# Kernel tuning notes

Hardware: AMD Instinct MI355X
Metric: run time of the kernel (lower is better)

## Reference

```python
import jax, jax.numpy as jnp
import numpy as np
from jax import lax


def setup_inputs() -> dict:
    key = jax.random.key(0)
    ks = jax.random.split(key, 6)
    B, T, F, C = 32, 256, 64, 16
    CO, P, S, K = 16, 64, 32, 4
    x = jax.random.normal(ks[0], (B, T, F, C), dtype=jnp.float32)
    static = jax.random.normal(ks[1], (B, S), dtype=jnp.float32)
    conv_w = jax.random.normal(ks[2], (F, CO, C, K), dtype=jnp.float32) * (1.0 / np.sqrt(C * K))
    conv_b = jax.random.normal(ks[3], (F, CO), dtype=jnp.float32) * 0.01
    W_p = jax.random.normal(ks[4], (F * C + S, P), dtype=jnp.float32) * (1.0 / np.sqrt(F * C + S))
    b_p = jax.random.normal(ks[5], (P,), dtype=jnp.float32) * 0.01
    return {"x": x, "static": static, "conv_w": conv_w, "conv_b": conv_b,
            "W_p": W_p, "b_p": b_p, "dilation": 2}


def _tpc_forward(x, static, conv_w, conv_b, W_p, b_p, dilation):
    B, T, F, C = x.shape
    _, CO, _, K = conv_w.shape
    left_pad = dilation * (K - 1)
    # --- feature-wise causal temporal conv as one grouped dilated conv ---
    # [B, T, F, C] -> [B, F*C, T]  (NCH layout)
    xr = x.transpose(0, 2, 3, 1).reshape(B, F * C, T)
    kr = conv_w.reshape(F * CO, C, K)  # groups = F
    y = lax.conv_general_dilated(
        xr, kr,
        window_strides=(1,),
        padding=[(left_pad, 0)],  # causal left padding
        rhs_dilation=(dilation,),
        dimension_numbers=("NCH", "OIH", "NCH"),
        feature_group_count=F,
    )  # [B, F*CO, T]
    temp_out = y.reshape(B, F, CO, T).transpose(0, 3, 1, 2) + conv_b[None, None, :, :]
    # --- pointwise branch on flattened features + static ---
    flat_x = x.reshape(B, T, F * C)
    static_rep = jnp.broadcast_to(static[:, None, :], (B, T, static.shape[-1]))
    point_in = jnp.concatenate([flat_x, static_rep], axis=-1)  # [B, T, F*C+S]
    point_out = point_in @ W_p + b_p  # [B, T, P]
    point_bcast = jnp.broadcast_to(point_out[:, :, None, :], (B, T, F, point_out.shape[-1]))
    # --- concat fusion + ReLU ---
    fused = jnp.concatenate([x, temp_out, point_bcast], axis=-1)
    return jax.nn.relu(fused)


def reference(x, static, conv_w, conv_b, W_p, b_p, dilation):
    return _tpc_forward(x, static, conv_w, conv_b, W_p, b_p, dilation)
```

## Files before the change

### kernel.cpp

```cpp
#include <hip/hip_runtime.h>

#define B_  32
#define T_  256
#define F_  64
#define C_  16
#define CO_ 16
#define P_  64
#define S_  32
#define K_  4
#define FC_ 1024
#define OUTC 96
#define TT  8
#define NS  14

typedef float floatx4 __attribute__((ext_vector_type(4)));

#define BARRIER_LGKM() asm volatile("s_waitcnt lgkmcnt(0)\n\ts_barrier" ::: "memory")

__global__ __launch_bounds__(512, 4) void tpc_fused(
    const float* __restrict__ x, const float* __restrict__ stat,
    const float* __restrict__ cw, const float* __restrict__ cb,
    const float* __restrict__ Wp, const float* __restrict__ bp,
    float* __restrict__ out)
{
    __shared__ __align__(16) float xs[NS * FC_];
    __shared__ __align__(16) float u[4096];

    int tid = threadIdx.x;
    int blk = blockIdx.x;
    int b  = blk >> 5;
    int t0 = (blk & 31) * TT;

    #pragma unroll
    for (int it = 0; it < 7; ++it) {
        int v = it * 512 + tid;
        int slice = v >> 8;
        int pos   = v & 255;
        int tg = t0 - 6 + slice;
        float4 val = make_float4(0.f, 0.f, 0.f, 0.f);
        if (tg >= 0)
            val = *(const float4*)(x + ((size_t)(b * T_ + tg)) * FC_ + pos * 4);
        *(float4*)(xs + slice * FC_ + pos * 4) = val;
    }
    __syncthreads();

    {
        int p  = tid & 63;
        int ks = tid >> 6;
        float acc[TT];
        #pragma unroll
        for (int r = 0; r < TT; ++r) acc[r] = 0.f;
        int k0base = ks * 128;
        for (int kk = 0; kk < 128; kk += 4) {
            int k0 = k0base + kk;
            float w0 = Wp[(size_t)(k0 + 0) * P_ + p];
            float w1 = Wp[(size_t)(k0 + 1) * P_ + p];
            float w2 = Wp[(size_t)(k0 + 2) * P_ + p];
            float w3 = Wp[(size_t)(k0 + 3) * P_ + p];
            #pragma unroll
            for (int r = 0; r < TT; ++r) {
                float4 xv = *(const float4*)(xs + (6 + r) * FC_ + k0);
                acc[r] += xv.x * w0 + xv.y * w1 + xv.z * w2 + xv.w * w3;
            }
        }
        #pragma unroll
        for (int r = 0; r < TT; ++r)
            u[(ks * TT + r) * P_ + p] = acc[r];
    }
    __syncthreads();

    {
        int p = tid & 63;
        int r = tid >> 6;
        float s = bp[p];
        const float* wst = Wp + (size_t)FC_ * P_;
        #pragma unroll 8
        for (int si = 0; si < S_; ++si)
            s += stat[b * S_ + si] * wst[si * P_ + p];
        #pragma unroll
        for (int ks = 0; ks < 8; ++ks)
            s += u[(ks * TT + r) * P_ + p];
        __syncthreads();
        u[3072 + r * P_ + p] = fmaxf(s, 0.f);
    }
    __syncthreads();

    int co = tid & 15;
    int fh = tid >> 4;
    int p  = tid & 63;
    int fg = tid >> 6;

    #pragma unroll
    for (int half = 0; half < 2; ++half) {
        int f = half * 32 + fh;
        float w[64];
        const float4* wg = (const float4*)(cw + ((size_t)(f * CO_ + co)) * (C_ * K_));
        #pragma unroll
        for (int j = 0; j < 16; ++j) {
            float4 t4 = wg[j];
            w[4 * j + 0] = t4.x; w[4 * j + 1] = t4.y;
            w[4 * j + 2] = t4.z; w[4 * j + 3] = t4.w;
        }
        float bias = cb[f * CO_ + co];

        for (int tl = 0; tl < TT; ++tl) {
            float temp = bias;
            #pragma unroll
            for (int k = 0; k < K_; ++k) {
                const float* sp = xs + (tl + 2 * k) * FC_ + f * C_;
                #pragma unroll
                for (int c4 = 0; c4 < 4; ++c4) {
                    float4 xv = *(const float4*)(sp + c4 * 4);
                    temp += xv.x * w[(c4 * 4 + 0) * 4 + k];
                    temp += xv.y * w[(c4 * 4 + 1) * 4 + k];
                    temp += xv.z * w[(c4 * 4 + 2) * 4 + k];
                    temp += xv.w * w[(c4 * 4 + 3) * 4 + k];
                }
            }
            u[fh * OUTC + 16 + co] = fmaxf(temp, 0.f);
            u[fh * OUTC + co] = fmaxf(xs[(tl + 6) * FC_ + f * C_ + co], 0.f);
            float pvv = u[3072 + tl * P_ + p];
            #pragma unroll
            for (int fo = 0; fo < 4; ++fo)
                u[(fo * 8 + fg) * OUTC + 32 + p] = pvv;
            BARRIER_LGKM();
            {
                const floatx4* src = (const floatx4*)u;
                floatx4* dst = (floatx4*)(out + ((size_t)(b * T_ + t0 + tl)) * F_ * OUTC
                                          + half * 3072);
                __builtin_nontemporal_store(src[tid], &dst[tid]);
                if (tid < 256)
                    __builtin_nontemporal_store(src[512 + tid], &dst[512 + tid]);
            }
            BARRIER_LGKM();
        }
    }
}

extern "C" void kernel_launch(void* const* d_in, const int* in_sizes, int n_in,
                              void* d_out, int out_size, void* d_ws, size_t ws_size,
                              hipStream_t stream) {
    const float* x    = (const float*)d_in[0];
    const float* stat = (const float*)d_in[1];
    const float* cw   = (const float*)d_in[2];
    const float* cb   = (const float*)d_in[3];
    const float* Wp   = (const float*)d_in[4];
    const float* bp   = (const float*)d_in[5];
    float* out = (float*)d_out;

    tpc_fused<<<1024, 512, 0, stream>>>(x, stat, cw, cb, Wp, bp, out);
}
```

Before: 279.4 us.

## Hoist pointwise-branch stores and reuse x slices across timesteps in conv

The broadcast pointwise outputs are now written straight to global memory in a separate pass, so they no longer go through shared memory once per timestep. The conv loop is restructured to load each of the 14 x slices once and scatter them into 8 per-timestep accumulators, which removes redundant LDS reads. Staging of the x/temp channels now alternates between two buffers, so only one barrier per timestep is needed. The trade-offs are higher register pressure from the 8 accumulators, and output rows that are written as separated 32-float and 64-float segments instead of contiguous 96-float rows.

```diff
diff --git a/kernel.cpp b/kernel.cpp
--- a/kernel.cpp
+++ b/kernel.cpp
@@ -85,10 +85,19 @@
     }
     __syncthreads();
 
+    {
+        int pp = tid & 15;
+        int fq = tid >> 4;
+        for (int tl = 0; tl < TT; ++tl) {
+            floatx4 v4 = *(const floatx4*)(u + 3072 + tl * P_ + pp * 4);
+            float* ob = out + ((size_t)(b * T_ + t0 + tl)) * F_ * OUTC + 32 + pp * 4;
+            __builtin_nontemporal_store(v4, (floatx4*)(ob + (size_t)fq * OUTC));
+            __builtin_nontemporal_store(v4, (floatx4*)(ob + (size_t)(32 + fq) * OUTC));
+        }
+    }
+
     int co = tid & 15;
     int fh = tid >> 4;
-    int p  = tid & 63;
-    int fg = tid >> 6;
 
     #pragma unroll
     for (int half = 0; half < 2; ++half) {
@@ -103,36 +112,45 @@
         }
         float bias = cb[f * CO_ + co];
 
-        for (int tl = 0; tl < TT; ++tl) {
-            float temp = bias;
+        float acc[TT];
+        #pragma unroll
+        for (int r = 0; r < TT; ++r) acc[r] = bias;
+
+        #pragma unroll
+        for (int s = 0; s < NS; ++s) {
+            const float* sp = xs + s * FC_ + f * C_;
+            float4 xv0 = *(const float4*)(sp + 0);
+            float4 xv1 = *(const float4*)(sp + 4);
+            float4 xv2 = *(const float4*)(sp + 8);
+            float4 xv3 = *(const float4*)(sp + 12);
             #pragma unroll
             for (int k = 0; k < K_; ++k) {
-                const float* sp = xs + (tl + 2 * k) * FC_ + f * C_;
-                #pragma unroll
-                for (int c4 = 0; c4 < 4; ++c4) {
-                    float4 xv = *(const float4*)(sp + c4 * 4);
-                    temp += xv.x * w[(c4 * 4 + 0) * 4 + k];
-                    temp += xv.y * w[(c4 * 4 + 1) * 4 + k];
-                    temp += xv.z * w[(c4 * 4 + 2) * 4 + k];
-                    temp += xv.w * w[(c4 * 4 + 3) * 4 + k];
-                }
+                int tl = s - 2 * k;
+                if (tl < 0 || tl >= TT) continue;
+                acc[tl] += xv0.x * w[0 * 4 + k];  acc[tl] += xv0.y * w[1 * 4 + k];
+                acc[tl] += xv0.z * w[2 * 4 + k];  acc[tl] += xv0.w * w[3 * 4 + k];
+                acc[tl] += xv1.x * w[4 * 4 + k];  acc[tl] += xv1.y * w[5 * 4 + k];
+                acc[tl] += xv1.z * w[6 * 4 + k];  acc[tl] += xv1.w * w[7 * 4 + k];
+                acc[tl] += xv2.x * w[8 * 4 + k];  acc[tl] += xv2.y * w[9 * 4 + k];
+                acc[tl] += xv2.z * w[10 * 4 + k]; acc[tl] += xv2.w * w[11 * 4 + k];
+                acc[tl] += xv3.x * w[12 * 4 + k]; acc[tl] += xv3.y * w[13 * 4 + k];
+                acc[tl] += xv3.z * w[14 * 4 + k]; acc[tl] += xv3.w * w[15 * 4 + k];
             }
-            u[fh * OUTC + 16 + co] = fmaxf(temp, 0.f);
-            u[fh * OUTC + co] = fmaxf(xs[(tl + 6) * FC_ + f * C_ + co], 0.f);
-            float pvv = u[3072 + tl * P_ + p];
-            #pragma unroll
-            for (int fo = 0; fo < 4; ++fo)
-                u[(fo * 8 + fg) * OUTC + 32 + p] = pvv;
+        }
+
+        for (int tl = 0; tl < TT; ++tl) {
+            float* buf = u + (tl & 1) * 1024;
+            buf[fh * 32 + 16 + co] = fmaxf(acc[tl], 0.f);
+            buf[fh * 32 + co] = fmaxf(xs[(tl + 6) * FC_ + f * C_ + co], 0.f);
             BARRIER_LGKM();
-            {
-                const floatx4* src = (const floatx4*)u;
-                floatx4* dst = (floatx4*)(out + ((size_t)(b * T_ + t0 + tl)) * F_ * OUTC
-                                          + half * 3072);
-                __builtin_nontemporal_store(src[tid], &dst[tid]);
-                if (tid < 256)
-                    __builtin_nontemporal_store(src[512 + tid], &dst[512 + tid]);
+            if (tid < 256) {
+                int fl = tid >> 3;
+                int q  = tid & 7;
+                floatx4 v = *(const floatx4*)(buf + fl * 32 + q * 4);
+                float* dst = out + ((size_t)(b * T_ + t0 + tl)) * F_ * OUTC
+                             + (size_t)(half * 32 + fl) * OUTC + q * 4;
+                __builtin_nontemporal_store(v, (floatx4*)dst);
             }
-            BARRIER_LGKM();
         }
     }
 }
```

Result: slower. 541.5 us (+93.8%).

## Store input tile and conv weights as bf16 in shared memory/registers

Applied to the files above, without the earlier changes.

Packs the staged x tile into bf16 pairs in LDS, halving shared memory use from about 56KB to 28KB, and packs the conv weights into bf16 pairs in registers. The aim is to raise occupancy and cut LDS traffic and register pressure. The passthrough x channels are re-read in fp32 from global memory so that part stays exact. The cost is rounding error from bf16 inputs and weights in both the conv and the pointwise matmul, plus extra unpack ALU work.

```diff
diff --git a/kernel.cpp b/kernel.cpp
--- a/kernel.cpp
+++ b/kernel.cpp
@@ -17,13 +17,21 @@
 
 #define BARRIER_LGKM() asm volatile("s_waitcnt lgkmcnt(0)\n\ts_barrier" ::: "memory")
 
+__device__ __forceinline__ unsigned pk2(float a, float b) {
+    unsigned ua = (__float_as_uint(a) + 0x8000u) >> 16;
+    unsigned ub = (__float_as_uint(b) + 0x8000u) >> 16;
+    return ua | (ub << 16);
+}
+__device__ __forceinline__ float lo16(unsigned w) { return __uint_as_float(w << 16); }
+__device__ __forceinline__ float hi16(unsigned w) { return __uint_as_float(w & 0xFFFF0000u); }
+
 __global__ __launch_bounds__(512, 4) void tpc_fused(
     const float* __restrict__ x, const float* __restrict__ stat,
     const float* __restrict__ cw, const float* __restrict__ cb,
     const float* __restrict__ Wp, const float* __restrict__ bp,
     float* __restrict__ out)
 {
-    __shared__ __align__(16) float xs[NS * FC_];
+    __shared__ __align__(16) unsigned xh[NS * 512];
     __shared__ __align__(16) float u[4096];
 
     int tid = threadIdx.x;
@@ -40,7 +48,10 @@
         float4 val = make_float4(0.f, 0.f, 0.f, 0.f);
         if (tg >= 0)
             val = *(const float4*)(x + ((size_t)(b * T_ + tg)) * FC_ + pos * 4);
-        *(float4*)(xs + slice * FC_ + pos * 4) = val;
+        uint2 pw;
+        pw.x = pk2(val.x, val.y);
+        pw.y = pk2(val.z, val.w);
+        *(uint2*)(xh + slice * 512 + pos * 2) = pw;
     }
     __syncthreads();
 
@@ -50,17 +61,25 @@
         float acc[TT];
         #pragma unroll
         for (int r = 0; r < TT; ++r) acc[r] = 0.f;
-        int k0base = ks * 128;
-        for (int kk = 0; kk < 128; kk += 4) {
-            int k0 = k0base + kk;
-            float w0 = Wp[(size_t)(k0 + 0) * P_ + p];
-            float w1 = Wp[(size_t)(k0 + 1) * P_ + p];
-            float w2 = Wp[(size_t)(k0 + 2) * P_ + p];
-            float w3 = Wp[(size_t)(k0 + 3) * P_ + p];
+        int kw0 = ks * 64;
+        for (int oct = 0; oct < 16; ++oct) {
+            int wi = kw0 + oct * 4;
+            int ke = ks * 128 + oct * 8;
+            float wv0 = Wp[(size_t)(ke + 0) * P_ + p];
+            float wv1 = Wp[(size_t)(ke + 1) * P_ + p];
+            float wv2 = Wp[(size_t)(ke + 2) * P_ + p];
+            float wv3 = Wp[(size_t)(ke + 3) * P_ + p];
+            float wv4 = Wp[(size_t)(ke + 4) * P_ + p];
+            float wv5 = Wp[(size_t)(ke + 5) * P_ + p];
+            float wv6 = Wp[(size_t)(ke + 6) * P_ + p];
+            float wv7 = Wp[(size_t)(ke + 7) * P_ + p];
             #pragma unroll
             for (int r = 0; r < TT; ++r) {
-                float4 xv = *(const float4*)(xs + (6 + r) * FC_ + k0);
-                acc[r] += xv.x * w0 + xv.y * w1 + xv.z * w2 + xv.w * w3;
+                uint4 q = *(const uint4*)(xh + (6 + r) * 512 + wi);
+                acc[r] += lo16(q.x) * wv0 + hi16(q.x) * wv1
+                        + lo16(q.y) * wv2 + hi16(q.y) * wv3
+                        + lo16(q.z) * wv4 + hi16(q.z) * wv5
+                        + lo16(q.w) * wv6 + hi16(q.w) * wv7;
             }
         }
         #pragma unroll
@@ -93,32 +112,38 @@
     #pragma unroll
     for (int half = 0; half < 2; ++half) {
         int f = half * 32 + fh;
-        float w[64];
+        unsigned wp2[32];
         const float4* wg = (const float4*)(cw + ((size_t)(f * CO_ + co)) * (C_ * K_));
         #pragma unroll
         for (int j = 0; j < 16; ++j) {
             float4 t4 = wg[j];
-            w[4 * j + 0] = t4.x; w[4 * j + 1] = t4.y;
-            w[4 * j + 2] = t4.z; w[4 * j + 3] = t4.w;
+            wp2[j * 2 + 0] = pk2(t4.x, t4.y);
+            wp2[j * 2 + 1] = pk2(t4.z, t4.w);
         }
         float bias = cb[f * CO_ + co];
 
         for (int tl = 0; tl < TT; ++tl) {
-            float temp = bias;
+            float a = bias;
             #pragma unroll
             for (int k = 0; k < K_; ++k) {
-                const float* sp = xs + (tl + 2 * k) * FC_ + f * C_;
-                #pragma unroll
-                for (int c4 = 0; c4 < 4; ++c4) {
-                    float4 xv = *(const float4*)(sp + c4 * 4);
-                    temp += xv.x * w[(c4 * 4 + 0) * 4 + k];
-                    temp += xv.y * w[(c4 * 4 + 1) * 4 + k];
-                    temp += xv.z * w[(c4 * 4 + 2) * 4 + k];
-                    temp += xv.w * w[(c4 * 4 + 3) * 4 + k];
-                }
+                const unsigned* sp = xh + (tl + 2 * k) * 512 + f * 8;
+                uint4 qa = *(const uint4*)sp;
+                uint4 qb = *(const uint4*)(sp + 4);
+                int h = k >> 1;
+                #define WK(c) ((k & 1) ? hi16(wp2[(c)*2 + h]) : lo16(wp2[(c)*2 + h]))
+                a += lo16(qa.x) * WK(0)  + hi16(qa.x) * WK(1);
+                a += lo16(qa.y) * WK(2)  + hi16(qa.y) * WK(3);
+                a += lo16(qa.z) * WK(4)  + hi16(qa.z) * WK(5);
+                a += lo16(qa.w) * WK(6)  + hi16(qa.w) * WK(7);
+                a += lo16(qb.x) * WK(8)  + hi16(qb.x) * WK(9);
+                a += lo16(qb.y) * WK(10) + hi16(qb.y) * WK(11);
+                a += lo16(qb.z) * WK(12) + hi16(qb.z) * WK(13);
+                a += lo16(qb.w) * WK(14) + hi16(qb.w) * WK(15);
+                #undef WK
             }
-            u[fh * OUTC + 16 + co] = fmaxf(temp, 0.f);
-            u[fh * OUTC + co] = fmaxf(xs[(tl + 6) * FC_ + f * C_ + co], 0.f);
+            float xg = x[((size_t)(b * T_ + t0 + tl) * F_ + f) * C_ + co];
+            u[fh * OUTC + 16 + co] = fmaxf(a, 0.f);
+            u[fh * OUTC + co] = fmaxf(xg, 0.f);
             float pvv = u[3072 + tl * P_ + p];
             #pragma unroll
             for (int fo = 0; fo < 4; ++fo)
```

New measurement: 288.7 us. +3.3%, slower.
